# Optimization experiments

Hardware: AMD Instinct MI355X
Metric: run time of the kernel (lower is better)

The kernel has to match this reference:

```python
import jax, jax.numpy as jnp
import numpy as np

N, E, F_IN = 50000, 800000, 256
H, C = 4, 64            # heads, per-head channels; H*C == 256
OUT = 64
NEG_SLOPE = 0.2


def _gat_conv(x, src, dst, W, a_src, a_dst, b):
    """PyG-style GATConv (concat=True, add_self_loops already applied in src/dst)."""
    n = x.shape[0]
    h = (x @ W).reshape(n, H, C)                      # [N,H,C]
    al_s = jnp.sum(h * a_src, axis=-1)                # [N,H]
    al_d = jnp.sum(h * a_dst, axis=-1)                # [N,H]
    e = jax.nn.leaky_relu(al_s[src] + al_d[dst], NEG_SLOPE)   # [E,H]
    # segment softmax over incoming edges of each dst node
    emax = jax.ops.segment_max(e, dst, num_segments=n)
    ee = jnp.exp(e - emax[dst])
    denom = jax.ops.segment_sum(ee, dst, num_segments=n)
    alpha = ee / denom[dst]                           # [E,H]
    msg = alpha[:, :, None] * h[src]                  # [E,H,C]
    out = jax.ops.segment_sum(msg, dst, num_segments=n)
    return out.reshape(n, H * C) + b


def setup_inputs() -> dict:
    key = jax.random.key(0)
    ks = jax.random.split(key, 12)
    x = jax.random.normal(ks[0], (N, F_IN), dtype=jnp.float32)
    edge_index = jax.random.randint(ks[1], (2, E), 0, N, dtype=jnp.int64)
    batch = jnp.zeros((N,), dtype=jnp.int64)

    def glorot(k, shape):
        fan = shape[0]
        return jax.random.normal(k, shape, dtype=jnp.float32) / jnp.sqrt(jnp.float32(fan))

    params = {
        "W1": glorot(ks[2], (F_IN, H * C)),
        "a_src1": jax.random.normal(ks[3], (H, C), dtype=jnp.float32) * 0.1,
        "a_dst1": jax.random.normal(ks[4], (H, C), dtype=jnp.float32) * 0.1,
        "b1": jnp.zeros((H * C,), dtype=jnp.float32),
        "W2": glorot(ks[5], (H * C, H * C)),
        "a_src2": jax.random.normal(ks[6], (H, C), dtype=jnp.float32) * 0.1,
        "a_dst2": jax.random.normal(ks[7], (H, C), dtype=jnp.float32) * 0.1,
        "b2": jnp.zeros((H * C,), dtype=jnp.float32),
        "fcW": glorot(ks[8], (H * C, OUT)),
        "fcb": jnp.zeros((OUT,), dtype=jnp.float32),
    }
    return {"x": x, "edge_index": edge_index, "batch": batch, **params}


def reference(x, edge_index, batch, W1, a_src1, a_dst1, b1, W2, a_src2, a_dst2, b2, fcW, fcb):
    n = x.shape[0]
    # PyG GATConv default add_self_loops=True
    loop = jnp.arange(n, dtype=edge_index.dtype)
    src = jnp.concatenate([edge_index[0], loop])
    dst = jnp.concatenate([edge_index[1], loop])

    h = jax.nn.elu(_gat_conv(x, src, dst, W1, a_src1, a_dst1, b1))
    h = jax.nn.elu(_gat_conv(h, src, dst, W2, a_src2, a_dst2, b2))
    # dropout is identity in eval mode; node_level=True -> no pooling
    logits = h @ fcW + fcb
    return logits
```

## Files before the change

kernel.cpp:

```cpp
#include <hip/hip_runtime.h>
#include <hip/hip_bf16.h>


#define HEADS 4
#define FDIM  256

typedef __attribute__((ext_vector_type(4))) float f32x4;
typedef __attribute__((ext_vector_type(8))) short s16x8;

__device__ __forceinline__ void gload_lds16(const void* g, void* l) {
    __builtin_amdgcn_global_load_lds(
        (__attribute__((address_space(1))) void*)g,
        (__attribute__((address_space(3))) void*)l, 16, 0, 0);
}

__device__ __forceinline__ float b2f(unsigned short u) {
    return __uint_as_float((unsigned)u << 16);
}
__device__ __forceinline__ unsigned short f2b(float f) {
    __hip_bfloat16 b = __float2bfloat16(f);
    return *(unsigned short*)&b;
}

__device__ __forceinline__ float fast_exp2(float t) {
#if __has_builtin(__builtin_amdgcn_exp2f)
    return __builtin_amdgcn_exp2f(t);
#else
    return __expf(t * 0.6931471805599453f);
#endif
}

__global__ void deg_hist(const int* __restrict__ dstp, int* __restrict__ deg,
                         int E, int Et) {
    int e = blockIdx.x * 256 + threadIdx.x;
    if (e >= Et) return;
    int dd = (e < E) ? dstp[e] : (e - E);
    atomicAdd(&deg[dd], 1);
}

__global__ void cvt_scan(const float* __restrict__ x, unsigned short* __restrict__ xb,
                         const float* __restrict__ W1, unsigned short* __restrict__ Wt1,
                         const float* __restrict__ W2, unsigned short* __restrict__ Wt2,
                         const float* __restrict__ fcW, unsigned short* __restrict__ fcWt,
                         const int* __restrict__ deg, int* __restrict__ offs,
                         int* __restrict__ cursor,
                         int nx4, int n, int cvtblocks) {
    if ((int)blockIdx.x >= cvtblocks) {
        __shared__ int red[4];
        __shared__ int wsums[4];
        __shared__ int base_sh;
        const int tid = threadIdx.x, lane = tid & 63, wv = tid >> 6;
        const int sid = (int)blockIdx.x - cvtblocks;
        const int start = sid * 256;

        int base = 0;
        for (int i = tid * 4; i < start; i += 1024) {
            int4 v = *(const int4*)(deg + i);
            base += v.x + v.y + v.z + v.w;
        }
#pragma unroll
        for (int m = 1; m < 64; m <<= 1) base += __shfl_xor(base, m, 64);
        if (lane == 0) red[wv] = base;
        __syncthreads();
        if (tid == 0) base_sh = red[0] + red[1] + red[2] + red[3];

        const int i = start + tid;
        int v = (i < n) ? deg[i] : 0;
        int acc = v;
#pragma unroll
        for (int d = 1; d < 64; d <<= 1) {
            int t = __shfl_up(acc, d, 64);
            if (lane >= d) acc += t;
        }
        if (lane == 63) wsums[wv] = acc;
        __syncthreads();
        int wo = 0;
#pragma unroll
        for (int k = 0; k < 4; ++k) wo += (k < wv) ? wsums[k] : 0;
        if (i < n) {
            int o = base_sh + wo + acc - v;
            offs[i] = o;
            cursor[i] = o;
        }
        return;
    }

    int i = blockIdx.x * 256 + threadIdx.x;
    if (i < nx4) {
        float4 v = ((const float4*)x)[i];
        ushort4 o;
        o.x = f2b(v.x); o.y = f2b(v.y); o.z = f2b(v.z); o.w = f2b(v.w);
        ((ushort4*)xb)[i] = o;
        return;
    }
    i -= nx4;
    if (i < FDIM * FDIM) {
        int r = i >> 8, c = i & 255;
        Wt1[c * FDIM + r] = f2b(W1[i]);
        return;
    }
    i -= FDIM * FDIM;
    if (i < FDIM * FDIM) {
        int r = i >> 8, c = i & 255;
        Wt2[c * FDIM + r] = f2b(W2[i]);
        return;
    }
    i -= FDIM * FDIM;
    if (i < FDIM * 64) {
        int r = i >> 6, c = i & 63;
        fcWt[c * FDIM + r] = f2b(fcW[i]);
    }
}

template <int BN, bool F32OUT, bool ATT, bool SCAT>
__global__ __launch_bounds__(256, 2)
void gemm_bt_k256(const unsigned short* __restrict__ A,
                  const unsigned short* __restrict__ Bt,
                  void* __restrict__ C,
                  const float* __restrict__ bias,
                  const float* __restrict__ a_src,
                  const float* __restrict__ a_dst,
                  float* __restrict__ als,
                  float* __restrict__ ald,
                  int M, int ncol,
                  const int* __restrict__ sc_src,
                  const int* __restrict__ sc_dst,
                  int* __restrict__ cursor,
                  int* __restrict__ csrs,
                  int E, int n) {
    constexpr int BM = 128, BK = 64;
    constexpr int NFRAG = BN / 32;
    constexpr int YNUM = (BN == 128) ? 2 : 1;
    __shared__ __align__(16) unsigned short lA[BM * BK];
    __shared__ __align__(16) unsigned short lB[BN * BK];

    const int mb = (M + 127) >> 7;
    const int nwg = mb * YNUM;
    int bid = blockIdx.x;

    if constexpr (SCAT) {
        if (bid >= nwg) {
            int e = (bid - nwg) * 256 + (int)threadIdx.x;
            const int Et = E + n;
            if (e < Et) {
                int s, dd;
                if (e < E) { s = sc_src[e]; dd = sc_dst[e]; }
                else       { s = e - E;     dd = s; }
                int p = atomicAdd(&cursor[dd], 1);
                csrs[p] = s;
            }
            return;
        }
    }

    {
        const int q = nwg >> 3, r = nwg & 7;
        const int xcd = bid & 7, sub = bid >> 3;
        bid = (xcd < r ? xcd * (q + 1) : r * (q + 1) + (xcd - r) * q) + sub;
    }
    const int gy = (YNUM == 2) ? (bid & 1) : 0;
    const int gx = (YNUM == 2) ? (bid >> 1) : bid;

    const int tid  = threadIdx.x;
    const int lane = tid & 63;
    const int wave = tid >> 6;
    const int wm = wave & 1, wn = wave >> 1;
    const int m0 = gx * BM;
    const int n0 = gy * BN;
    const int quad = lane >> 4, col16 = lane & 15;

    f32x4 acc[4][NFRAG];
#pragma unroll
    for (int i = 0; i < 4; ++i)
#pragma unroll
        for (int j = 0; j < NFRAG; ++j) acc[i][j] = (f32x4){0.f, 0.f, 0.f, 0.f};

#pragma unroll 1
    for (int kt = 0; kt < 4; ++kt) {
        const int k0 = kt * BK;
#pragma unroll
        for (int i = 0; i < 4; ++i) {
            int slot = tid + i * 256;
            int row = slot >> 3, g = slot & 7;
            int gs = g ^ (row & 7);
            int rg = m0 + row; rg = rg < M ? rg : (M - 1);
            gload_lds16(A + (size_t)rg * FDIM + k0 + gs * 8,
                        (char*)lA + (size_t)slot * 16);
        }
#pragma unroll
        for (int i = 0; i < BN * 8 / 256; ++i) {
            int slot = tid + i * 256;
            int row = slot >> 3, g = slot & 7;
            int gs = g ^ (row & 7);
            gload_lds16(Bt + (size_t)(n0 + row) * FDIM + k0 + gs * 8,
                        (char*)lB + (size_t)slot * 16);
        }
        __syncthreads();

#pragma unroll
        for (int kk = 0; kk < 2; ++kk) {
            const int kg = kk * 4 + quad;
            s16x8 af[4], bfr[NFRAG];
#pragma unroll
            for (int i = 0; i < 4; ++i) {
                int row = wm * 64 + i * 16 + col16;
                int g = kg ^ (row & 7);
                af[i] = *(const s16x8*)((const char*)lA + (size_t)(row * 8 + g) * 16);
            }
#pragma unroll
            for (int j = 0; j < NFRAG; ++j) {
                int row = wn * (BN / 2) + j * 16 + col16;
                int g = kg ^ (row & 7);
                bfr[j] = *(const s16x8*)((const char*)lB + (size_t)(row * 8 + g) * 16);
            }
#pragma unroll
            for (int i = 0; i < 4; ++i)
#pragma unroll
                for (int j = 0; j < NFRAG; ++j)
                    acc[i][j] = __builtin_amdgcn_mfma_f32_16x16x32_bf16(
                        af[i], bfr[j], acc[i][j], 0, 0, 0);
        }
        __syncthreads();
    }

#pragma unroll
    for (int i = 0; i < 4; ++i) {
#pragma unroll
        for (int j = 0; j < NFRAG; ++j) {
#pragma unroll
            for (int r = 0; r < 4; ++r) {
                int row = m0 + wm * 64 + i * 16 + quad * 4 + r;
                int col = n0 + wn * (BN / 2) + j * 16 + col16;
                if (row < M) {
                    float v = acc[i][j][r];
                    if (bias) v += bias[col];
                    if constexpr (F32OUT)
                        ((float*)C)[(size_t)row * ncol + col] = v;
                    else
                        ((unsigned short*)C)[(size_t)row * ncol + col] = f2b(v);
                }
            }
        }
    }

    if constexpr (ATT) {
        constexpr float LOG2E = 1.4426950408889634f;
        const int head = gy * 2 + wn;
        float asv[4], adv[4];
#pragma unroll
        for (int j = 0; j < 4; ++j) {
            int c = head * 64 + j * 16 + col16;
            asv[j] = a_src[c] * LOG2E;
            adv[j] = a_dst[c] * LOG2E;
        }
#pragma unroll
        for (int i = 0; i < 4; ++i) {
#pragma unroll
            for (int r = 0; r < 4; ++r) {
                float vs = acc[i][0][r] * asv[0] + acc[i][1][r] * asv[1]
                         + acc[i][2][r] * asv[2] + acc[i][3][r] * asv[3];
                float vd = acc[i][0][r] * adv[0] + acc[i][1][r] * adv[1]
                         + acc[i][2][r] * adv[2] + acc[i][3][r] * adv[3];
#pragma unroll
                for (int m = 1; m < 16; m <<= 1) {
                    vs += __shfl_xor(vs, m, 16);
                    vd += __shfl_xor(vd, m, 16);
                }
                int row = m0 + wm * 64 + i * 16 + quad * 4 + r;
                if (col16 == 0 && row < M) {
                    als[row * HEADS + head] = vs;
                    ald[row * HEADS + head] = vd;
                }
            }
        }
    }
}

__global__ void gat_gather(const int* __restrict__ off,
                           const int* __restrict__ deg,
                           const int* __restrict__ csr_src,
                           const float* __restrict__ als,
                           const float* __restrict__ ald,
                           const unsigned short* __restrict__ h,
                           const float* __restrict__ bias,
                           unsigned short* __restrict__ x2, int n) {
    const int lane = threadIdx.x & 63;
    const int d = (blockIdx.x * blockDim.x + threadIdx.x) >> 6;
    if (d >= n) return;
    const int head = lane >> 4;
    const float aldh = ald[4 * d + head];
    const int start = off[d];
    const int end = start + deg[d];

    float a0 = 0.f, a1 = 0.f, a2 = 0.f, a3 = 0.f, den = 0.f;
    int j = start;
    for (; j + 8 <= end; j += 8) {
        int s[8];
#pragma unroll
        for (int u = 0; u < 8; ++u) s[u] = csr_src[j + u];
        float e[8];
#pragma unroll
        for (int u = 0; u < 8; ++u) e[u] = als[4 * s[u] + head];
        ushort4 hv[8];
#pragma unroll
        for (int u = 0; u < 8; ++u)
            hv[u] = *(const ushort4*)(h + (size_t)s[u] * FDIM + lane * 4);
#pragma unroll
        for (int u = 0; u < 8; ++u) {
            float t = e[u] + aldh;
            t = t > 0.f ? t : 0.2f * t;
            float w = fast_exp2(t);
            den += w;
            a0 += w * b2f(hv[u].x);
            a1 += w * b2f(hv[u].y);
            a2 += w * b2f(hv[u].z);
            a3 += w * b2f(hv[u].w);
        }
    }
    for (; j + 4 <= end; j += 4) {
        int s[4];
#pragma unroll
        for (int u = 0; u < 4; ++u) s[u] = csr_src[j + u];
        float e[4];
#pragma unroll
        for (int u = 0; u < 4; ++u) e[u] = als[4 * s[u] + head];
        ushort4 hv[4];
#pragma unroll
        for (int u = 0; u < 4; ++u)
            hv[u] = *(const ushort4*)(h + (size_t)s[u] * FDIM + lane * 4);
#pragma unroll
        for (int u = 0; u < 4; ++u) {
            float t = e[u] + aldh;
            t = t > 0.f ? t : 0.2f * t;
            float w = fast_exp2(t);
            den += w;
            a0 += w * b2f(hv[u].x);
            a1 += w * b2f(hv[u].y);
            a2 += w * b2f(hv[u].z);
            a3 += w * b2f(hv[u].w);
        }
    }
    for (; j < end; ++j) {
        int s = csr_src[j];
        float t = als[4 * s + head] + aldh;
        t = t > 0.f ? t : 0.2f * t;
        float w = fast_exp2(t);
        ushort4 hv = *(const ushort4*)(h + (size_t)s * FDIM + lane * 4);
        den += w;
        a0 += w * b2f(hv.x);
        a1 += w * b2f(hv.y);
        a2 += w * b2f(hv.z);
        a3 += w * b2f(hv.w);
    }
    const float inv = 1.0f / den;
    const int c = lane * 4;
    float v0 = a0 * inv + bias[c + 0];
    float v1 = a1 * inv + bias[c + 1];
    float v2 = a2 * inv + bias[c + 2];
    float v3 = a3 * inv + bias[c + 3];
    v0 = v0 > 0.f ? v0 : expm1f(v0);
    v1 = v1 > 0.f ? v1 : expm1f(v1);
    v2 = v2 > 0.f ? v2 : expm1f(v2);
    v3 = v3 > 0.f ? v3 : expm1f(v3);
    ushort4 o;
    o.x = f2b(v0); o.y = f2b(v1); o.z = f2b(v2); o.w = f2b(v3);
    *(ushort4*)(x2 + (size_t)d * FDIM + c) = o;
}

extern "C" void kernel_launch(void* const* d_in, const int* in_sizes, int n_in,
                              void* d_out, int out_size, void* d_ws, size_t ws_size,
                              hipStream_t stream) {
    const float* x   = (const float*)d_in[0];
    const int*   ei  = (const int*)d_in[1];
    const float* W1  = (const float*)d_in[3];
    const float* as1 = (const float*)d_in[4];
    const float* ad1 = (const float*)d_in[5];
    const float* b1  = (const float*)d_in[6];
    const float* W2  = (const float*)d_in[7];
    const float* as2 = (const float*)d_in[8];
    const float* ad2 = (const float*)d_in[9];
    const float* b2  = (const float*)d_in[10];
    const float* fcW = (const float*)d_in[11];
    const float* fcb = (const float*)d_in[12];
    float* out = (float*)d_out;

    const int n = in_sizes[0] / FDIM;
    const int E = in_sizes[1] / 2;
    const int Etot = E + n;
    const int* srcp = ei;
    const int* dstp = ei + E;
    const int nb = (n + 255) / 256;

    char* ws = (char*)d_ws;
    size_t off_b = 0;
    auto carve = [&](size_t bytes) -> char* {
        char* p = ws + off_b;
        off_b += (bytes + 255) & ~(size_t)255;
        return p;
    };
    unsigned short* xb = (unsigned short*)carve((size_t)n * FDIM * 2);
    unsigned short* h  = (unsigned short*)carve((size_t)n * FDIM * 2);
    float* als  = (float*)carve((size_t)n * HEADS * 4);
    float* ald  = (float*)carve((size_t)n * HEADS * 4);
    int* deg    = (int*)carve((size_t)n * 4);
    int* offs   = (int*)carve((size_t)(n + 1) * 4);
    int* cursor = (int*)carve((size_t)n * 4);
    int* csr_src = (int*)carve((size_t)Etot * 4);
    unsigned short* Wt1  = (unsigned short*)carve(FDIM * FDIM * 2);
    unsigned short* Wt2  = (unsigned short*)carve(FDIM * FDIM * 2);
    unsigned short* fcWt = (unsigned short*)carve(64 * FDIM * 2);
    unsigned short* x2 = xb;

    const int mblocks = (n + 127) / 128;
    const int nx4 = n * FDIM / 4;
    const int cvtblocks = (nx4 + 2 * FDIM * FDIM + FDIM * 64 + 255) / 256;
    const int SB = (Etot + 255) / 256;

    hipMemsetAsync(deg, 0, (size_t)n * 4, stream);

    deg_hist<<<(Etot + 255) / 256, 256, 0, stream>>>(dstp, deg, E, Etot);

    cvt_scan<<<cvtblocks + nb, 256, 0, stream>>>(
        x, xb, W1, Wt1, W2, Wt2, fcW, fcWt, deg, offs, cursor,
        nx4, n, cvtblocks);

    gemm_bt_k256<128, false, true, true><<<mblocks * 2 + SB, 256, 0, stream>>>(
        xb, Wt1, h, nullptr, as1, ad1, als, ald, n, FDIM,
        srcp, dstp, cursor, csr_src, E, n);
    gat_gather<<<(n + 3) / 4, 256, 0, stream>>>(
        offs, deg, csr_src, als, ald, h, b1, x2, n);

    gemm_bt_k256<128, false, true, false><<<mblocks * 2, 256, 0, stream>>>(
        x2, Wt2, h, nullptr, as2, ad2, als, ald, n, FDIM,
        nullptr, nullptr, nullptr, nullptr, 0, 0);
    gat_gather<<<(n + 3) / 4, 256, 0, stream>>>(
        offs, deg, csr_src, als, ald, h, b2, x2, n);

    gemm_bt_k256<64, true, false, false><<<mblocks, 256, 0, stream>>>(
        x2, fcWt, out, fcb, nullptr, nullptr, nullptr, nullptr, n, 64,
        nullptr, nullptr, nullptr, nullptr, 0, 0);
}
```

Before: 376.2 us.

## Build CSR via 32-node bucket histogram, bucket scatter, and per-bucket local sort

Replaces the per-node degree histogram and multi-block prefix scan with a bucket-level histogram over groups of 32 destination nodes. That histogram uses shared-memory atomics, and a single-wave scan turns it into bucket offsets. Edges are scattered into their buckets as packed (src, local dst) words, and a new csr_build kernel then locally sorts each bucket to produce the per-node offsets, degrees and CSR sources. The aim is to cut global atomic traffic and the redundant prefix reads of the old scan. In exchange it adds a kernel launch and an extra pass over the edges, concentrates the scatter atomics on far fewer counters, and packs source ids into 16 bits, which caps the node count at 65536.

```diff
diff --git a/kernel.cpp b/kernel.cpp
--- a/kernel.cpp
+++ b/kernel.cpp
@@ -4,6 +4,7 @@
 
 #define HEADS 4
 #define FDIM  256
+#define NBK_MAX 2048
 
 typedef __attribute__((ext_vector_type(4))) float f32x4;
 typedef __attribute__((ext_vector_type(8))) short s16x8;
@@ -30,57 +31,58 @@
 #endif
 }
 
-__global__ void deg_hist(const int* __restrict__ dstp, int* __restrict__ deg,
-                         int E, int Et) {
-    int e = blockIdx.x * 256 + threadIdx.x;
-    if (e >= Et) return;
-    int dd = (e < E) ? dstp[e] : (e - E);
-    atomicAdd(&deg[dd], 1);
+__global__ void bucket_hist(const int* __restrict__ dstp, int* __restrict__ bHist,
+                            int E, int Et, int nbk) {
+    __shared__ int lh[NBK_MAX];
+    const int tid = threadIdx.x;
+    for (int i = tid; i < NBK_MAX; i += blockDim.x) lh[i] = 0;
+    __syncthreads();
+    const int stride = gridDim.x * blockDim.x;
+    for (int e = blockIdx.x * blockDim.x + tid; e < Et; e += stride) {
+        int dd = (e < E) ? dstp[e] : (e - E);
+        atomicAdd(&lh[dd >> 5], 1);
+    }
+    __syncthreads();
+    for (int i = tid; i < nbk; i += blockDim.x)
+        if (lh[i]) atomicAdd(&bHist[i], lh[i]);
 }
 
 __global__ void cvt_scan(const float* __restrict__ x, unsigned short* __restrict__ xb,
                          const float* __restrict__ W1, unsigned short* __restrict__ Wt1,
                          const float* __restrict__ W2, unsigned short* __restrict__ Wt2,
                          const float* __restrict__ fcW, unsigned short* __restrict__ fcWt,
-                         const int* __restrict__ deg, int* __restrict__ offs,
-                         int* __restrict__ cursor,
-                         int nx4, int n, int cvtblocks) {
+                         const int* __restrict__ bHist, int* __restrict__ bOffs,
+                         int* __restrict__ bCur,
+                         int nx4, int nbk, int cvtblocks) {
     if ((int)blockIdx.x >= cvtblocks) {
-        __shared__ int red[4];
-        __shared__ int wsums[4];
-        __shared__ int base_sh;
-        const int tid = threadIdx.x, lane = tid & 63, wv = tid >> 6;
-        const int sid = (int)blockIdx.x - cvtblocks;
-        const int start = sid * 256;
-
-        int base = 0;
-        for (int i = tid * 4; i < start; i += 1024) {
-            int4 v = *(const int4*)(deg + i);
-            base += v.x + v.y + v.z + v.w;
-        }
-#pragma unroll
-        for (int m = 1; m < 64; m <<= 1) base += __shfl_xor(base, m, 64);
-        if (lane == 0) red[wv] = base;
-        __syncthreads();
-        if (tid == 0) base_sh = red[0] + red[1] + red[2] + red[3];
-
-        const int i = start + tid;
-        int v = (i < n) ? deg[i] : 0;
-        int acc = v;
-#pragma unroll
-        for (int d = 1; d < 64; d <<= 1) {
-            int t = __shfl_up(acc, d, 64);
-            if (lane >= d) acc += t;
-        }
-        if (lane == 63) wsums[wv] = acc;
-        __syncthreads();
-        int wo = 0;
-#pragma unroll
-        for (int k = 0; k < 4; ++k) wo += (k < wv) ? wsums[k] : 0;
-        if (i < n) {
-            int o = base_sh + wo + acc - v;
-            offs[i] = o;
-            cursor[i] = o;
+        const int tid = threadIdx.x;
+        if (tid < 64) {
+            const int base = tid * 32;
+            int vals[32];
+            int s = 0;
+#pragma unroll
+            for (int k = 0; k < 32; ++k) {
+                int idx = base + k;
+                int v = (idx < nbk) ? bHist[idx] : 0;
+                vals[k] = s;
+                s += v;
+            }
+            int acc = s;
+#pragma unroll
+            for (int d = 1; d < 64; d <<= 1) {
+                int t = __shfl_up(acc, d, 64);
+                if (tid >= d) acc += t;
+            }
+            const int pre = acc - s;
+#pragma unroll
+            for (int k = 0; k < 32; ++k) {
+                int idx = base + k;
+                if (idx <= nbk) {
+                    int o = pre + vals[k];
+                    bOffs[idx] = o;
+                    if (idx < nbk) bCur[idx] = o;
+                }
+            }
         }
         return;
     }
@@ -109,6 +111,48 @@
     if (i < FDIM * 64) {
         int r = i >> 6, c = i & 63;
         fcWt[c * FDIM + r] = f2b(fcW[i]);
+    }
+}
+
+__global__ void csr_build(const unsigned int* __restrict__ pairs,
+                          const int* __restrict__ bOffs,
+                          int* __restrict__ offs, int* __restrict__ deg,
+                          int* __restrict__ csr_src, int n) {
+    __shared__ int hist[32], loc[32], lcur[32];
+    const int b = blockIdx.x;
+    const int tid = threadIdx.x;
+    const int rb = bOffs[b], re = bOffs[b + 1];
+
+    if (tid < 32) hist[tid] = 0;
+    __syncthreads();
+    for (int i = rb + tid; i < re; i += 128) {
+        unsigned p = pairs[i];
+        atomicAdd(&hist[(p >> 16) & 31], 1);
+    }
+    __syncthreads();
+    if (tid < 32) {
+        int v = hist[tid];
+        int a = v;
+#pragma unroll
+        for (int d = 1; d < 32; d <<= 1) {
+            int t = __shfl_up(a, d, 32);
+            if (tid >= d) a += t;
+        }
+        int lo = a - v;
+        loc[tid] = lo;
+        lcur[tid] = 0;
+        int node = b * 32 + tid;
+        if (node < n) {
+            offs[node] = rb + lo;
+            deg[node] = v;
+        }
+    }
+    __syncthreads();
+    for (int i = rb + tid; i < re; i += 128) {
+        unsigned p = pairs[i];
+        int dl = (p >> 16) & 31;
+        int pos = atomicAdd(&lcur[dl], 1);
+        csr_src[rb + loc[dl] + pos] = (int)(p & 0xFFFFu);
     }
 }
 
@@ -125,8 +169,8 @@
                   int M, int ncol,
                   const int* __restrict__ sc_src,
                   const int* __restrict__ sc_dst,
-                  int* __restrict__ cursor,
-                  int* __restrict__ csrs,
+                  int* __restrict__ bCur,
+                  unsigned int* __restrict__ pairs,
                   int E, int n) {
     constexpr int BM = 128, BK = 64;
     constexpr int NFRAG = BN / 32;
@@ -146,8 +190,8 @@
                 int s, dd;
                 if (e < E) { s = sc_src[e]; dd = sc_dst[e]; }
                 else       { s = e - E;     dd = s; }
-                int p = atomicAdd(&cursor[dd], 1);
-                csrs[p] = s;
+                int p = atomicAdd(&bCur[dd >> 5], 1);
+                pairs[p] = (unsigned)s | ((unsigned)(dd & 31) << 16);
             }
             return;
         }
@@ -389,7 +433,7 @@
     const int Etot = E + n;
     const int* srcp = ei;
     const int* dstp = ei + E;
-    const int nb = (n + 255) / 256;
+    const int nbk = (n + 31) / 32;
 
     char* ws = (char*)d_ws;
     size_t off_b = 0;
@@ -404,7 +448,10 @@
     float* ald  = (float*)carve((size_t)n * HEADS * 4);
     int* deg    = (int*)carve((size_t)n * 4);
     int* offs   = (int*)carve((size_t)(n + 1) * 4);
-    int* cursor = (int*)carve((size_t)n * 4);
+    int* bHist  = (int*)carve((size_t)NBK_MAX * 4);
+    int* bOffs  = (int*)carve((size_t)(NBK_MAX + 1) * 4);
+    int* bCur   = (int*)carve((size_t)NBK_MAX * 4);
+    unsigned int* pairs = (unsigned int*)carve((size_t)Etot * 4);
     int* csr_src = (int*)carve((size_t)Etot * 4);
     unsigned short* Wt1  = (unsigned short*)carve(FDIM * FDIM * 2);
     unsigned short* Wt2  = (unsigned short*)carve(FDIM * FDIM * 2);
@@ -416,17 +463,20 @@
     const int cvtblocks = (nx4 + 2 * FDIM * FDIM + FDIM * 64 + 255) / 256;
     const int SB = (Etot + 255) / 256;
 
-    hipMemsetAsync(deg, 0, (size_t)n * 4, stream);
-
-    deg_hist<<<(Etot + 255) / 256, 256, 0, stream>>>(dstp, deg, E, Etot);
-
-    cvt_scan<<<cvtblocks + nb, 256, 0, stream>>>(
-        x, xb, W1, Wt1, W2, Wt2, fcW, fcWt, deg, offs, cursor,
-        nx4, n, cvtblocks);
+    hipMemsetAsync(bHist, 0, (size_t)nbk * 4, stream);
+
+    bucket_hist<<<128, 1024, 0, stream>>>(dstp, bHist, E, Etot, nbk);
+
+    cvt_scan<<<cvtblocks + 1, 256, 0, stream>>>(
+        x, xb, W1, Wt1, W2, Wt2, fcW, fcWt, bHist, bOffs, bCur,
+        nx4, nbk, cvtblocks);
 
     gemm_bt_k256<128, false, true, true><<<mblocks * 2 + SB, 256, 0, stream>>>(
         xb, Wt1, h, nullptr, as1, ad1, als, ald, n, FDIM,
-        srcp, dstp, cursor, csr_src, E, n);
+        srcp, dstp, bCur, pairs, E, n);
+
+    csr_build<<<nbk, 128, 0, stream>>>(pairs, bOffs, offs, deg, csr_src, n);
+
     gat_gather<<<(n + 3) / 4, 256, 0, stream>>>(
         offs, deg, csr_src, als, ald, h, b1, x2, n);
 
```

Measured after the change: 434.3 us. +15.4%, slower.
